# Kernel optimization log

Measured on AMD Instinct MI355X. Metric: run time of the kernel, lower is better.

The kernel has to match this reference:

```python
import jax, jax.numpy as jnp
import numpy as np

V, D, NL, K, B, L, FF = 32000, 512, 4, 32, 2, 1024, 2048


def _ln(x, g, b, eps=1e-5):
    m = jnp.mean(x, axis=-1, keepdims=True)
    v = jnp.mean((x - m) ** 2, axis=-1, keepdims=True)
    return (x - m) * jax.lax.rsqrt(v + eps) * g + b


def setup_inputs() -> dict:
    key = jax.random.key(0)
    ks = jax.random.split(key, 16)
    s = 0.02
    n = lambda k, shape: jax.random.normal(k, shape, jnp.float32) * s
    inp = {
        "tokens": jax.random.randint(ks[0], (B, L), 0, V),
        "embed": n(ks[1], (V, D)),
        "ln1_g": jnp.ones((NL, D)), "ln1_b": jnp.zeros((NL, D)),
        "cp_w1": n(ks[2], (NL, D, D)), "cp_b1": jnp.zeros((NL, D)),
        "cp_w2": n(ks[3], (NL, D, K)), "cp_b2": jnp.zeros((NL, K)),
        "pos_scale": 0.5 * jnp.ones((NL,)), "content_scale": 0.5 * jnp.ones((NL,)),
        "val_w": n(ks[4], (NL, D, D)), "val_b": jnp.zeros((NL, D)),
        "oln_g": jnp.ones((NL, D)), "oln_b": jnp.zeros((NL, D)),
        "out_w": n(ks[5], (NL, D, D)), "out_b": jnp.zeros((NL, D)),
        "ln2_g": jnp.ones((NL, D)), "ln2_b": jnp.zeros((NL, D)),
        "ffn_w1": n(ks[6], (NL, D, FF)), "ffn_b1": jnp.zeros((NL, FF)),
        "ffn_w2": n(ks[7], (NL, FF, D)), "ffn_b2": jnp.zeros((NL, D)),
        "no_g": jnp.ones((D,)), "no_b": jnp.zeros((D,)),
        "head_b": jnp.zeros((V,)),
    }
    return inp


def _forward(tokens, embed, ln1_g, ln1_b, cp_w1, cp_b1, cp_w2, cp_b2,
             pos_scale, content_scale, val_w, val_b, oln_g, oln_b, out_w, out_b,
             ln2_g, ln2_b, ffn_w1, ffn_b1, ffn_w2, ffn_b2, no_g, no_b, head_b):
    Bn, Ln = tokens.shape
    Kn = cp_b2.shape[1]
    # fixed positional phases (register_buffer in torch)
    freqs = 1.0 / 10000.0 ** (jnp.arange(Kn, dtype=jnp.float32) / Kn)
    pos_phase = jnp.arange(Ln, dtype=jnp.float32)[:, None] * freqs[None, :]  # [L,K]
    inv_norm = 1.0 / jnp.sqrt(jnp.arange(1, Ln + 1, dtype=jnp.float32) * Kn)[None, :, None]
    h = embed[tokens]  # [B,L,D]
    for i in range(ln1_g.shape[0]):
        # --- DualAddressingPhasor on normed input ---
        x = _ln(h, ln1_g[i], ln1_b[i])
        cp = jnp.tanh(jnp.tanh(x @ cp_w1[i] + cp_b1[i]) @ cp_w2[i] + cp_b2[i]) * jnp.pi  # [B,L,K]
        tp = pos_scale[i] * pos_phase[None] + content_scale[i] * cp
        v = x @ val_w[i] + val_b[i]  # [B,L,D]
        c, s_ = jnp.cos(tp), jnp.sin(tp)  # [B,L,K]
        mem_r = jnp.cumsum(c[..., None] * v[:, :, None, :], axis=1)  # [B,L,K,D]
        mem_i = jnp.cumsum(s_[..., None] * v[:, :, None, :], axis=1)
        retrieved = (jnp.einsum('blkd,blk->bld', mem_r, c)
                     + jnp.einsum('blkd,blk->bld', mem_i, s_)) * inv_norm
        # phasor returns x + to_out(retrieved); block adds it back to h
        h = h + x + (_ln(retrieved, oln_g[i], oln_b[i]) @ out_w[i] + out_b[i])
        # --- FFN ---
        y = _ln(h, ln2_g[i], ln2_b[i])
        h = h + jax.nn.gelu(y @ ffn_w1[i] + ffn_b1[i], approximate=False) @ ffn_w2[i] + ffn_b2[i]
    # tied output head: head.weight = embed.weight
    return _ln(h, no_g, no_b) @ embed.T + head_b


def reference(tokens, embed, ln1_g, ln1_b, cp_w1, cp_b1, cp_w2, cp_b2,
              pos_scale, content_scale, val_w, val_b, oln_g, oln_b, out_w, out_b,
              ln2_g, ln2_b, ffn_w1, ffn_b1, ffn_w2, ffn_b2, no_g, no_b, head_b):
    return _forward(tokens, embed, ln1_g, ln1_b, cp_w1, cp_b1, cp_w2, cp_b2,
                    pos_scale, content_scale, val_w, val_b, oln_g, oln_b, out_w, out_b,
                    ln2_g, ln2_b, ffn_w1, ffn_b1, ffn_w2, ffn_b2, no_g, no_b, head_b)
```

## Files before the change

### kernel.cpp

```cpp
#include <hip/hip_runtime.h>
#include <hip/hip_bf16.h>
#include <math.h>

#define V_  32000
#define D_  512
#define NL_ 4
#define K_  32
#define B_  2
#define L_  1024
#define FF_ 2048
#define MR_ (B_ * L_)

typedef __bf16 bf16_t;
typedef __bf16 bf16x8 __attribute__((ext_vector_type(8)));
typedef float  f32x4  __attribute__((ext_vector_type(4)));

#define FLAG_TANH   1
#define FLAG_GELU   2
#define FLAG_INV    8
#define FLAG_CAUSAL 16
#define FLAG_TANHLO 32
#define FLAG_TRI    64
#define FLAG_HALFK  128

#define GLDS(gsrc, ldst) \
  __builtin_amdgcn_global_load_lds( \
      (const __attribute__((address_space(1))) unsigned int*)(const void*)(gsrc), \
      (__attribute__((address_space(3))) unsigned int*)(void*)(ldst), 16, 0, 0)

__global__ void gather_kernel(const int* __restrict__ tokens,
                              const float* __restrict__ embed,
                              float* __restrict__ h) {
    int row = blockIdx.x;
    int t = tokens[row];
    const float4* src = (const float4*)(embed + (size_t)t * D_);
    float4* dst = (float4*)(h + (size_t)row * D_);
    dst[threadIdx.x] = src[threadIdx.x];
}

__global__ __launch_bounds__(256) void cvt_kernel(const float* __restrict__ in,
                                                  bf16_t* __restrict__ out) {
    size_t i = ((size_t)blockIdx.x * 256 + threadIdx.x) * 8;
    float4 f0 = ((const float4*)(in + i))[0];
    float4 f1 = ((const float4*)(in + i))[1];
    bf16x8 ov;
    ov[0] = (bf16_t)f0.x; ov[1] = (bf16_t)f0.y;
    ov[2] = (bf16_t)f0.z; ov[3] = (bf16_t)f0.w;
    ov[4] = (bf16_t)f1.x; ov[5] = (bf16_t)f1.y;
    ov[6] = (bf16_t)f1.z; ov[7] = (bf16_t)f1.w;
    *(bf16x8*)(out + i) = ov;
}

__global__ void bconcat_kernel(const float* __restrict__ a,
                               const float* __restrict__ b,
                               float* __restrict__ o) {
    int i = blockIdx.x, t = threadIdx.x;
    o[(size_t)i * 2 * D_ + t]       = a[(size_t)i * D_ + t];
    o[(size_t)i * 2 * D_ + D_ + t]  = b[(size_t)i * D_ + t];
}

__global__ __launch_bounds__(256) void ln_kernel(const float* __restrict__ in,
                                                 const float* __restrict__ g,
                                                 const float* __restrict__ b,
                                                 float* __restrict__ outf,
                                                 bf16_t* __restrict__ outb) {
    int row = blockIdx.x, tid = threadIdx.x;
    const float* rp = in + (size_t)row * D_;
    float v0 = rp[tid], v1 = rp[tid + 256];
    float s = v0 + v1, q = v0 * v0 + v1 * v1;
#pragma unroll
    for (int o = 32; o > 0; o >>= 1) {
        s += __shfl_down(s, o, 64);
        q += __shfl_down(q, o, 64);
    }
    __shared__ float ss[4], sq[4];
    if ((tid & 63) == 0) { ss[tid >> 6] = s; sq[tid >> 6] = q; }
    __syncthreads();
    float ts = ss[0] + ss[1] + ss[2] + ss[3];
    float tq = sq[0] + sq[1] + sq[2] + sq[3];
    float mean = ts * (1.0f / D_);
    float var = tq * (1.0f / D_) - mean * mean;
    float rstd = rsqrtf(var + 1e-5f);
    float o0 = (v0 - mean) * rstd * g[tid] + b[tid];
    float o1 = (v1 - mean) * rstd * g[tid + 256] + b[tid + 256];
    if (outf) {
        outf[(size_t)row * D_ + tid]       = o0;
        outf[(size_t)row * D_ + tid + 256] = o1;
    }
    if (outb) {
        outb[(size_t)row * D_ + tid]       = (bf16_t)o0;
        outb[(size_t)row * D_ + tid + 256] = (bf16_t)o1;
    }
}

__global__ __launch_bounds__(256) void sumk_ln_kernel(
    const float* __restrict__ p0, const float* __restrict__ p1,
    const float* __restrict__ bias, float* __restrict__ h,
    const float* __restrict__ g, const float* __restrict__ b,
    float* __restrict__ outf, bf16_t* __restrict__ outb) {
    int row = blockIdx.x, tid = threadIdx.x;
    size_t o = (size_t)row * D_;
    float v0 = h[o + tid]       + p0[o + tid]       + p1[o + tid]       + bias[tid];
    float v1 = h[o + tid + 256] + p0[o + tid + 256] + p1[o + tid + 256] + bias[tid + 256];
    h[o + tid]       = v0;
    h[o + tid + 256] = v1;
    float s = v0 + v1, q = v0 * v0 + v1 * v1;
#pragma unroll
    for (int of = 32; of > 0; of >>= 1) {
        s += __shfl_down(s, of, 64);
        q += __shfl_down(q, of, 64);
    }
    __shared__ float ss[4], sq[4];
    if ((tid & 63) == 0) { ss[tid >> 6] = s; sq[tid >> 6] = q; }
    __syncthreads();
    float ts = ss[0] + ss[1] + ss[2] + ss[3];
    float tq = sq[0] + sq[1] + sq[2] + sq[3];
    float mean = ts * (1.0f / D_);
    float var = tq * (1.0f / D_) - mean * mean;
    float rstd = rsqrtf(var + 1e-5f);
    float o0 = (v0 - mean) * rstd * g[tid] + b[tid];
    float o1 = (v1 - mean) * rstd * g[tid + 256] + b[tid + 256];
    if (outf) {
        outf[o + tid]       = o0;
        outf[o + tid + 256] = o1;
    }
    outb[o + tid]       = (bf16_t)o0;
    outb[o + tid + 256] = (bf16_t)o1;
}

__global__ __launch_bounds__(256) void tconv_kernel(const float* __restrict__ in,
                                                    bf16_t* __restrict__ out,
                                                    int R, int C,
                                                    size_t inz, size_t outz) {
    __shared__ float t[32][33];
    const float* ip = in + (size_t)blockIdx.z * inz;
    bf16_t* op = out + (size_t)blockIdx.z * outz;
    int r0 = blockIdx.y * 32, c0 = blockIdx.x * 32;
    int tx = threadIdx.x & 31, ty = threadIdx.x >> 5;
#pragma unroll
    for (int rr = 0; rr < 4; ++rr)
        t[ty + rr * 8][tx] = ip[(size_t)(r0 + ty + rr * 8) * C + c0 + tx];
    __syncthreads();
#pragma unroll
    for (int rr = 0; rr < 4; ++rr)
        op[(size_t)(c0 + ty + rr * 8) * R + r0 + tx] = (bf16_t)t[tx][ty + rr * 8];
}

template<int BM, int BN, int NBUF, int BK, bool BF32>
__global__ __launch_bounds__(256) void mgemm(
    const bf16_t* __restrict__ A, const void* __restrict__ Bp,
    const float* __restrict__ bias, const float* __restrict__ res1,
    const float* __restrict__ res2, float* __restrict__ Cf,
    bf16_t* __restrict__ Cb, int M, int N, int Kd, int flags,
    long long strA, long long strB, long long strC, int swz) {
    __shared__ bf16_t sA[NBUF][BM * BK];
    __shared__ bf16_t sB[NBUF][BN * BK];
    const int tid = threadIdx.x;
    const int wave = tid >> 6, lane = tid & 63;
    const int lrow = lane & 15, quad = lane >> 4;
    int bx = blockIdx.x, by = blockIdx.y;
    if (swz) {
        int gx = gridDim.x, gy = gridDim.y;
        int nwg = gx * gy;
        int lid = by * gx + bx;
        int q = nwg >> 3, r = nwg & 7;
        int xcd = lid & 7, slot = lid >> 3;
        int base = (xcd < r) ? xcd * (q + 1) : r * (q + 1) + (xcd - r) * q;
        int nid = base + slot;
        bx = nid / gy;
        by = nid - bx * gy;
    }
    if ((flags & FLAG_TRI) && bx > by) return;
    const int m0 = by * BM, n0 = bx * BN;
    const int z = blockIdx.z;
    A += (size_t)z * strA;
    const bf16_t* Bb = (const bf16_t*)Bp + (BF32 ? 0 : (size_t)z * strB);
    const float*  Bf = (const float*)Bp  + (BF32 ? (size_t)z * strB : 0);
    constexpr int TM = BM / 32, TN = BN / 32;
    const int wm = (wave >> 1) * (BM / 2), wn = (wave & 1) * (BN / 2);
    f32x4 acc[TM][TN] = {};

    if constexpr (BF32) {
        for (int k0 = 0; k0 < Kd; k0 += 32) {
#pragma unroll
            for (int rb = 0; rb < BM / 64; ++rb) {
                int rowblk = wave * (BM / 64) + rb;
                int ml = rowblk * 16 + (lane >> 2);
                int qs = (lane & 3) ^ ((ml >> 1) & 3);
                GLDS(A + (size_t)(m0 + ml) * Kd + k0 + qs * 8, &sA[0][rowblk * 512]);
            }
#pragma unroll
            for (int rb = 0; rb < (BN * 4) / 256; ++rb) {
                int s = rb * 256 + tid;
                int nl = s >> 2, ql = s & 3;
                int qs = ql ^ ((nl >> 1) & 3);
                const float* src = Bf + (size_t)(n0 + nl) * Kd + k0 + qs * 8;
                float4 f0 = ((const float4*)src)[0];
                float4 f1 = ((const float4*)src)[1];
                bf16x8 ov;
                ov[0] = (bf16_t)f0.x; ov[1] = (bf16_t)f0.y;
                ov[2] = (bf16_t)f0.z; ov[3] = (bf16_t)f0.w;
                ov[4] = (bf16_t)f1.x; ov[5] = (bf16_t)f1.y;
                ov[6] = (bf16_t)f1.z; ov[7] = (bf16_t)f1.w;
                *(bf16x8*)(&sB[0][s * 8]) = ov;
            }
            __syncthreads();
            bf16x8 af[TM], bv[TN];
#pragma unroll
            for (int i = 0; i < TM; ++i) {
                int row = wm + i * 16 + lrow;
                af[i] = *(const bf16x8*)(&sA[0][(row * 4 + (quad ^ ((row >> 1) & 3))) * 8]);
            }
#pragma unroll
            for (int j = 0; j < TN; ++j) {
                int rown = wn + j * 16 + lrow;
                bv[j] = *(const bf16x8*)(&sB[0][(rown * 4 + (quad ^ ((rown >> 1) & 3))) * 8]);
            }
#pragma unroll
            for (int i = 0; i < TM; ++i)
#pragma unroll
                for (int j = 0; j < TN; ++j)
                    acc[i][j] = __builtin_amdgcn_mfma_f32_16x16x32_bf16(af[i], bv[j], acc[i][j], 0, 0, 0);
            __syncthreads();
        }
    } else if constexpr (BK == 64) {
        int kend = Kd;
        if (flags & FLAG_CAUSAL) { int ke = m0 + BM; kend = ke < Kd ? ke : Kd; }
        if (flags & FLAG_HALFK) kend = Kd >> 1;
        const int nk = kend >> 6;
        constexpr int NLD = BM / 32 + BN / 32;
        auto stage = [&](int t, int buf) {
            const int k0 = t << 6;
#pragma unroll
            for (int rb = 0; rb < BM / 32; ++rb) {
                int r0 = (wave * (BM / 32) + rb) * 8;
                int row = r0 + (lane >> 3);
                int cs_ = (lane & 7) ^ (row & 7);
                GLDS(A + (size_t)(m0 + row) * Kd + k0 + cs_ * 8, &sA[buf][r0 * 64]);
            }
#pragma unroll
            for (int rb = 0; rb < BN / 32; ++rb) {
                int r0 = (wave * (BN / 32) + rb) * 8;
                int row = r0 + (lane >> 3);
                int cs_ = (lane & 7) ^ (row & 7);
                GLDS(Bb + (size_t)(n0 + row) * Kd + k0 + cs_ * 8, &sB[buf][r0 * 64]);
            }
        };
        auto compute = [&](int buf) {
            const bf16_t* sAc = sA[buf];
            const bf16_t* sBc = sB[buf];
            bf16x8 a0[TM], a1[TM], b0[TN], b1[TN];
#pragma unroll
            for (int i = 0; i < TM; ++i) {
                int row = wm + i * 16 + lrow;
                a0[i] = *(const bf16x8*)(sAc + row * 64 + ((quad       ^ (row & 7)) * 8));
                a1[i] = *(const bf16x8*)(sAc + row * 64 + (((4 | quad) ^ (row & 7)) * 8));
            }
#pragma unroll
            for (int j = 0; j < TN; ++j) {
                int rown = wn + j * 16 + lrow;
                b0[j] = *(const bf16x8*)(sBc + rown * 64 + ((quad       ^ (rown & 7)) * 8));
                b1[j] = *(const bf16x8*)(sBc + rown * 64 + (((4 | quad) ^ (rown & 7)) * 8));
            }
#pragma unroll
            for (int i = 0; i < TM; ++i)
#pragma unroll
                for (int j = 0; j < TN; ++j)
                    acc[i][j] = __builtin_amdgcn_mfma_f32_16x16x32_bf16(a0[i], b0[j], acc[i][j], 0, 0, 0);
#pragma unroll
            for (int i = 0; i < TM; ++i)
#pragma unroll
                for (int j = 0; j < TN; ++j)
                    acc[i][j] = __builtin_amdgcn_mfma_f32_16x16x32_bf16(a1[i], b1[j], acc[i][j], 0, 0, 0);
        };
        for (int t = 0; t < NBUF - 1 && t < nk; ++t) stage(t, t);
        int bcur = 0;
        for (int t = 0; t < nk; ++t) {
            const int nxt = t + NBUF - 1;
            if (nxt < nk) {
                int bn = bcur + NBUF - 1; if (bn >= NBUF) bn -= NBUF;
                stage(nxt, bn);
            }
            const int last = (nxt < nk) ? nxt : nk - 1;
            const int ahead = last - t;
            if (ahead >= 2)      asm volatile("s_waitcnt vmcnt(%0)" :: "n"(2 * NLD) : "memory");
            else if (ahead == 1) asm volatile("s_waitcnt vmcnt(%0)" :: "n"(1 * NLD) : "memory");
            else                 asm volatile("s_waitcnt vmcnt(0)" ::: "memory");
            __builtin_amdgcn_s_barrier();
            compute(bcur);
            asm volatile("s_waitcnt lgkmcnt(0)" ::: "memory");
            __builtin_amdgcn_s_barrier();
            bcur = (bcur + 1 == NBUF) ? 0 : bcur + 1;
        }
    } else {
        int kend = Kd;
        if (flags & FLAG_CAUSAL) { int ke = m0 + BM; kend = ke < Kd ? ke : Kd; }
        if (flags & FLAG_HALFK) kend = Kd >> 1;
        const int nk = kend >> 5;
        constexpr int NLD = BM / 64 + BN / 64;
        auto stage = [&](int t, int buf) {
            const int k0 = t << 5;
#pragma unroll
            for (int rb = 0; rb < BM / 64; ++rb) {
                int rowblk = wave * (BM / 64) + rb;
                int ml = rowblk * 16 + (lane >> 2);
                int qs = (lane & 3) ^ ((ml >> 1) & 3);
                GLDS(A + (size_t)(m0 + ml) * Kd + k0 + qs * 8, &sA[buf][rowblk * 512]);
            }
#pragma unroll
            for (int rb = 0; rb < BN / 64; ++rb) {
                int rowblk = wave * (BN / 64) + rb;
                int nl = rowblk * 16 + (lane >> 2);
                int qs = (lane & 3) ^ ((nl >> 1) & 3);
                GLDS(Bb + (size_t)(n0 + nl) * Kd + k0 + qs * 8, &sB[buf][rowblk * 512]);
            }
            if constexpr (BN == 64) {
                int nl = wave * 16 + (lane >> 2);
                int qs = (lane & 3) ^ ((nl >> 1) & 3);
                GLDS(Bb + (size_t)(n0 + nl) * Kd + k0 + qs * 8, &sB[buf][wave * 512]);
            }
        };
        auto compute = [&](int buf) {
            const bf16_t* sAc = sA[buf];
            const bf16_t* sBc = sB[buf];
            bf16x8 af[TM], bv[TN];
#pragma unroll
            for (int i = 0; i < TM; ++i) {
                int row = wm + i * 16 + lrow;
                af[i] = *(const bf16x8*)(sAc + (row * 4 + (quad ^ ((row >> 1) & 3))) * 8);
            }
#pragma unroll
            for (int j = 0; j < TN; ++j) {
                int rown = wn + j * 16 + lrow;
                bv[j] = *(const bf16x8*)(sBc + (rown * 4 + (quad ^ ((rown >> 1) & 3))) * 8);
            }
#pragma unroll
            for (int i = 0; i < TM; ++i)
#pragma unroll
                for (int j = 0; j < TN; ++j)
                    acc[i][j] = __builtin_amdgcn_mfma_f32_16x16x32_bf16(af[i], bv[j], acc[i][j], 0, 0, 0);
        };
        constexpr int NLDE = NLD + (BN == 64 ? 1 : 0);
        if constexpr (NBUF == 2) {
            stage(0, 0);
            int cur = 0;
            for (int t = 0; t < nk; ++t) {
                if (t + 1 < nk) {
                    stage(t + 1, cur ^ 1);
                    asm volatile("s_waitcnt vmcnt(%0)" :: "n"(NLDE) : "memory");
                } else {
                    asm volatile("s_waitcnt vmcnt(0)" ::: "memory");
                }
                __builtin_amdgcn_s_barrier();
                compute(cur);
                asm volatile("s_waitcnt lgkmcnt(0)" ::: "memory");
                __builtin_amdgcn_s_barrier();
                cur ^= 1;
            }
        } else {
            stage(0, 0);
            if (nk > 1) stage(1, 1);
            int b0 = 0;
            for (int t = 0; t < nk; ++t) {
                const int nxt = t + 2;
                if (nxt < nk) {
                    int bn = b0 + 2; if (bn >= 3) bn -= 3;
                    stage(nxt, bn);
                }
                const int last = (nxt < nk) ? nxt : nk - 1;
                const int ahead = last - t;
                if (ahead >= 2)      asm volatile("s_waitcnt vmcnt(%0)" :: "n"(2 * NLDE) : "memory");
                else if (ahead == 1) asm volatile("s_waitcnt vmcnt(%0)" :: "n"(1 * NLDE) : "memory");
                else                 asm volatile("s_waitcnt vmcnt(0)" ::: "memory");
                __builtin_amdgcn_s_barrier();
                compute(b0);
                asm volatile("s_waitcnt lgkmcnt(0)" ::: "memory");
                __builtin_amdgcn_s_barrier();
                b0 = (b0 == 2) ? 0 : b0 + 1;
            }
        }
    }

    const size_t zo = (size_t)z * strC;
#pragma unroll
    for (int i = 0; i < TM; ++i) {
#pragma unroll
        for (int reg = 0; reg < 4; ++reg) {
            int m = m0 + wm + i * 16 + quad * 4 + reg;
            float rs = (flags & FLAG_INV) ? rsqrtf((float)(m + 1) * (float)K_) : 1.0f;
#pragma unroll
            for (int j = 0; j < TN; ++j) {
                int n = n0 + wn + j * 16 + lrow;
                float vv = acc[i][j][reg];
                if (bias) vv += bias[n];
                vv *= rs;
                if (flags & FLAG_TANH) vv = tanhf(vv);
                else if (flags & FLAG_GELU) vv = 0.5f * vv * (1.0f + erff(vv * 0.7071067811865476f));
                else if (flags & FLAG_TANHLO) { if (n < D_) vv = tanhf(vv); }
                if ((flags & FLAG_TRI) && n > m) vv = 0.f;
                size_t idx = zo + (size_t)m * N + n;
                if (res1) vv += res1[idx];
                if (res2) vv += res2[idx];
                if (Cf) Cf[idx] = vv;
                if (Cb) Cb[idx] = (bf16_t)vv;
            }
        }
    }
}

__global__ __launch_bounds__(256) void phase_kernel(const float* __restrict__ t1,
                             const float* __restrict__ w2,
                             const float* __restrict__ b2,
                             const float* __restrict__ ps,
                             const float* __restrict__ cs,
                             int layer,
                             bf16_t* __restrict__ csb) {
    int tid = threadIdx.x;
    int rl = tid >> 6;
    int k = tid & 31, hh = (tid >> 5) & 1;
    int row = blockIdx.x * 4 + rl;
    int l = row & (L_ - 1);
    const float* tr = t1 + (size_t)row * (2 * D_);
    float acc = 0.f;
    for (int d = hh * 256; d < hh * 256 + 256; ++d)
        acc = fmaf(tr[d], w2[d * K_ + k], acc);
    __shared__ float red[256];
    red[tid] = acc;
    __syncthreads();
    if (hh == 0) {
        float zz = red[rl * 64 + k] + red[rl * 64 + 32 + k] + b2[k];
        float cp = tanhf(zz) * 3.14159265358979323846f;
        float freq = expf(-(float)k * (9.210340371976184f / (float)K_));
        float tp = ps[layer] * (float)l * freq + cs[layer] * cp;
        csb[(size_t)row * 64 + k]      = (bf16_t)cosf(tp);
        csb[(size_t)row * 64 + 32 + k] = (bf16_t)sinf(tp);
    }
}

extern "C" void kernel_launch(void* const* d_in, const int* in_sizes, int n_in,
                              void* d_out, int out_size, void* d_ws, size_t ws_size,
                              hipStream_t stream) {
    const int*   tokens        = (const int*)d_in[0];
    const float* embed         = (const float*)d_in[1];
    const float* ln1_g         = (const float*)d_in[2];
    const float* ln1_b         = (const float*)d_in[3];
    const float* cp_w1         = (const float*)d_in[4];
    const float* cp_b1         = (const float*)d_in[5];
    const float* cp_w2         = (const float*)d_in[6];
    const float* cp_b2         = (const float*)d_in[7];
    const float* pos_scale     = (const float*)d_in[8];
    const float* content_scale = (const float*)d_in[9];
    const float* val_w         = (const float*)d_in[10];
    const float* val_b         = (const float*)d_in[11];
    const float* oln_g         = (const float*)d_in[12];
    const float* oln_b         = (const float*)d_in[13];
    const float* out_w         = (const float*)d_in[14];
    const float* out_b         = (const float*)d_in[15];
    const float* ln2_g         = (const float*)d_in[16];
    const float* ln2_b         = (const float*)d_in[17];
    const float* ffn_w1        = (const float*)d_in[18];
    const float* ffn_b1        = (const float*)d_in[19];
    const float* ffn_w2        = (const float*)d_in[20];
    const float* ffn_b2        = (const float*)d_in[21];
    const float* no_g          = (const float*)d_in[22];
    const float* no_b          = (const float*)d_in[23];
    const float* head_b        = (const float*)d_in[24];
    float* out = (float*)d_out;

    float* h   = out;
    float* x   = h  + (size_t)MR_ * D_;
    float* t1v = x  + (size_t)MR_ * D_;
    float* r   = t1v + (size_t)MR_ * 2 * D_;
    bf16_t* x_bf  = (bf16_t*)(r + (size_t)MR_ * D_);
    bf16_t* r_bf  = x_bf  + (size_t)MR_ * D_;
    bf16_t* y_bf  = r_bf  + (size_t)MR_ * D_;
    bf16_t* ff_bf = y_bf  + (size_t)MR_ * D_;
    bf16_t* sc_bf = ff_bf + (size_t)MR_ * FF_;
    bf16_t* vT_bf = sc_bf + (size_t)B_ * L_ * L_;
    bf16_t* csb   = vT_bf + (size_t)B_ * D_ * L_;
    bf16_t* wvT   = csb   + (size_t)MR_ * 64;
    bf16_t* owT   = wvT   + (size_t)NL_ * 2 * D_ * D_;
    bf16_t* f1T   = owT   + (size_t)NL_ * D_ * D_;
    bf16_t* f2T   = f1T   + (size_t)NL_ * FF_ * D_;
    float*  b1v   = (float*)(f2T + (size_t)NL_ * D_ * FF_);
    float*  pK    = b1v + (size_t)NL_ * 2 * D_;
    bf16_t* hn_bf = (bf16_t*)d_ws;
    bf16_t* emb_bf = hn_bf + (size_t)MR_ * D_;
    const bool big_ws =
        ws_size >= ((size_t)MR_ * D_ + (size_t)V_ * D_) * sizeof(bf16_t);

    gather_kernel<<<MR_, 128, 0, stream>>>(tokens, embed, h);

    tconv_kernel<<<dim3(16, 16, NL_), 256, 0, stream>>>(cp_w1, wvT, D_, D_, (size_t)D_ * D_, (size_t)2 * D_ * D_);
    tconv_kernel<<<dim3(16, 16, NL_), 256, 0, stream>>>(val_w, wvT + (size_t)D_ * D_, D_, D_, (size_t)D_ * D_, (size_t)2 * D_ * D_);
    bconcat_kernel<<<NL_, 512, 0, stream>>>(cp_b1, val_b, b1v);
    tconv_kernel<<<dim3(16, 16, NL_), 256, 0, stream>>>(out_w, owT, D_, D_, (size_t)D_ * D_, (size_t)D_ * D_);
    tconv_kernel<<<dim3(64, 16, NL_), 256, 0, stream>>>(ffn_w1, f1T, D_, FF_, (size_t)D_ * FF_, (size_t)D_ * FF_);
    tconv_kernel<<<dim3(16, 64, NL_), 256, 0, stream>>>(ffn_w2, f2T, FF_, D_, (size_t)FF_ * D_, (size_t)FF_ * D_);
    if (big_ws)
        cvt_kernel<<<(V_ * D_) / 2048, 256, 0, stream>>>(embed, emb_bf);

    for (int i = 0; i < NL_; ++i) {
        if (i == 0)
            ln_kernel<<<MR_, 256, 0, stream>>>(h, ln1_g, ln1_b, x, x_bf);
        mgemm<64, 64, 3, 64, false><<<dim3(16, 32, 1), 256, 0, stream>>>(
            x_bf, wvT + (size_t)i * 2 * D_ * D_, b1v + (size_t)i * 2 * D_,
            nullptr, nullptr, t1v, nullptr, MR_, 2 * D_, D_, FLAG_TANHLO, 0, 0, 0, 1);
        phase_kernel<<<MR_ / 4, 256, 0, stream>>>(
            t1v, cp_w2 + (size_t)i * D_ * K_, cp_b2 + i * K_,
            pos_scale, content_scale, i, csb);
        tconv_kernel<<<dim3(16, 32, B_), 256, 0, stream>>>(
            t1v + D_, vT_bf, L_, 2 * D_, (size_t)L_ * 2 * D_, (size_t)D_ * L_);
        mgemm<64, 64, 3, 64, false><<<dim3(L_ / 64, L_ / 64, B_), 256, 0, stream>>>(
            csb, csb, nullptr, nullptr, nullptr, nullptr, sc_bf,
            L_, L_, 64, FLAG_TRI,
            (long long)L_ * 64, (long long)L_ * 64, (long long)L_ * L_, 0);
        mgemm<64, 64, 3, 64, false><<<dim3(8, 16, B_), 256, 0, stream>>>(
            sc_bf, vT_bf, nullptr, nullptr, nullptr, r, nullptr,
            L_, D_, L_, FLAG_INV | FLAG_CAUSAL,
            (long long)L_ * L_, (long long)D_ * L_, (long long)L_ * D_, 1);
        ln_kernel<<<MR_, 256, 0, stream>>>(r, oln_g + i * D_, oln_b + i * D_, nullptr, r_bf);
        mgemm<64, 64, 3, 64, false><<<dim3(8, 32, 1), 256, 0, stream>>>(
            r_bf, owT + (size_t)i * D_ * D_, out_b + i * D_,
            h, x, h, nullptr, MR_, D_, D_, 0, 0, 0, 0, 1);
        ln_kernel<<<MR_, 256, 0, stream>>>(h, ln2_g + i * D_, ln2_b + i * D_, nullptr, y_bf);
        mgemm<64, 64, 3, 64, false><<<dim3(32, 32, 1), 256, 0, stream>>>(
            y_bf, f1T + (size_t)i * FF_ * D_, ffn_b1 + i * FF_,
            nullptr, nullptr, nullptr, ff_bf, MR_, FF_, D_, FLAG_GELU, 0, 0, 0, 1);
        mgemm<64, 64, 3, 64, false><<<dim3(8, 32, 2), 256, 0, stream>>>(
            ff_bf, f2T + (size_t)i * D_ * FF_, nullptr,
            nullptr, nullptr, pK, nullptr, MR_, D_, FF_, FLAG_HALFK,
            (long long)(FF_ / 2), (long long)(FF_ / 2), (long long)MR_ * D_, 1);
        if (i < NL_ - 1) {
            sumk_ln_kernel<<<MR_, 256, 0, stream>>>(
                pK, pK + (size_t)MR_ * D_, ffn_b2 + i * D_, h,
                ln1_g + (i + 1) * D_, ln1_b + (i + 1) * D_, x, x_bf);
        } else {
            sumk_ln_kernel<<<MR_, 256, 0, stream>>>(
                pK, pK + (size_t)MR_ * D_, ffn_b2 + i * D_, h,
                no_g, no_b, nullptr, hn_bf);
        }
    }

    if (big_ws) {
        mgemm<128, 64, 3, 32, false><<<dim3(V_ / 64, MR_ / 128, 1), 256, 0, stream>>>(
            hn_bf, emb_bf, head_b, nullptr, nullptr, out, nullptr,
            MR_, V_, D_, 0, 0, 0, 0, 1);
    } else {
        mgemm<128, 128, 1, 32, true><<<dim3(V_ / 128, MR_ / 128, 1), 256, 0, stream>>>(
            hn_bf, embed, head_b, nullptr, nullptr, out, nullptr,
            MR_, V_, D_, 0, 0, 0, 0, 1);
    }
}
```

Baseline: 1.318 ms.

## Fuse phasor score and value GEMMs into one flash-style causal attention kernel

Replaces the two-GEMM path (materialise the triangular LxL score matrix in bf16, then multiply by V) with a single kernel. Each block computes a 64x64 score tile in registers, masks it causally, stages it through shared memory, and accumulates it against V tiles, with the inverse-norm scaling done in the epilogue. This removes the global write and re-read of the score matrix and one launch per layer. The cost is recomputing score tiles once per D-tile (eight times), with a single-buffered loop that has no prefetching. Separately, the out-projection and FFN2 GEMMs switch to 64x32 tiles with twice as many blocks, to raise occupancy on the N=512 outputs.

```diff
diff --git a/kernel.cpp b/kernel.cpp
--- a/kernel.cpp
+++ b/kernel.cpp
@@ -144,6 +144,103 @@
 #pragma unroll
     for (int rr = 0; rr < 4; ++rr)
         op[(size_t)(c0 + ty + rr * 8) * R + r0 + tx] = (bf16_t)t[tx][ty + rr * 8];
+}
+
+__global__ __launch_bounds__(256) void phattn_kernel(
+    const bf16_t* __restrict__ csb,
+    const bf16_t* __restrict__ vT,
+    float* __restrict__ r) {
+    __shared__ bf16_t sQ[64 * 64];
+    __shared__ bf16_t sK[64 * 64];
+    __shared__ bf16_t sV[64 * 64];
+    __shared__ bf16_t sS[64][72];
+    const int tid = threadIdx.x;
+    const int wave = tid >> 6, lane = tid & 63;
+    const int lrow = lane & 15, quad = lane >> 4;
+    const int wm = (wave >> 1) * 32, wn = (wave & 1) * 32;
+    const int b = blockIdx.z;
+    const int m0 = blockIdx.y * 64, d0 = blockIdx.x * 64;
+    const bf16_t* cs = csb + (size_t)b * L_ * 64;
+    const bf16_t* vz = vT + (size_t)b * D_ * L_;
+#pragma unroll
+    for (int p = 0; p < 2; ++p) {
+        int s = p * 256 + tid;
+        int row = s >> 3, c8 = s & 7;
+        *(bf16x8*)(sQ + row * 64 + c8 * 8) =
+            *(const bf16x8*)(cs + (size_t)(m0 + row) * 64 + c8 * 8);
+    }
+    f32x4 racc[2][2] = {};
+    const int njt = (m0 >> 6) + 1;
+    for (int jt = 0; jt < njt; ++jt) {
+        const int j0 = jt * 64;
+        __syncthreads();
+#pragma unroll
+        for (int p = 0; p < 2; ++p) {
+            int s = p * 256 + tid;
+            int row = s >> 3, c8 = s & 7;
+            *(bf16x8*)(sK + row * 64 + c8 * 8) =
+                *(const bf16x8*)(cs + (size_t)(j0 + row) * 64 + c8 * 8);
+            *(bf16x8*)(sV + row * 64 + c8 * 8) =
+                *(const bf16x8*)(vz + (size_t)(d0 + row) * L_ + j0 + c8 * 8);
+        }
+        __syncthreads();
+        f32x4 sacc[2][2] = {};
+#pragma unroll
+        for (int ks = 0; ks < 2; ++ks) {
+            bf16x8 qa[2], kb[2];
+#pragma unroll
+            for (int i = 0; i < 2; ++i)
+                qa[i] = *(const bf16x8*)(sQ + (wm + i * 16 + lrow) * 64 + ks * 32 + quad * 8);
+#pragma unroll
+            for (int j = 0; j < 2; ++j)
+                kb[j] = *(const bf16x8*)(sK + (wn + j * 16 + lrow) * 64 + ks * 32 + quad * 8);
+#pragma unroll
+            for (int i = 0; i < 2; ++i)
+#pragma unroll
+                for (int j = 0; j < 2; ++j)
+                    sacc[i][j] = __builtin_amdgcn_mfma_f32_16x16x32_bf16(qa[i], kb[j], sacc[i][j], 0, 0, 0);
+        }
+#pragma unroll
+        for (int i = 0; i < 2; ++i)
+#pragma unroll
+            for (int reg = 0; reg < 4; ++reg)
+#pragma unroll
+                for (int j = 0; j < 2; ++j) {
+                    int mm = wm + i * 16 + quad * 4 + reg;
+                    int jj = wn + j * 16 + lrow;
+                    float vv = sacc[i][j][reg];
+                    if (j0 + jj > m0 + mm) vv = 0.f;
+                    sS[mm][jj] = (bf16_t)vv;
+                }
+        __syncthreads();
+#pragma unroll
+        for (int ks = 0; ks < 2; ++ks) {
+            bf16x8 pa[2], vb[2];
+#pragma unroll
+            for (int i = 0; i < 2; ++i)
+                pa[i] = *(const bf16x8*)(&sS[wm + i * 16 + lrow][ks * 32 + quad * 8]);
+#pragma unroll
+            for (int j = 0; j < 2; ++j)
+                vb[j] = *(const bf16x8*)(sV + (wn + j * 16 + lrow) * 64 + ks * 32 + quad * 8);
+#pragma unroll
+            for (int i = 0; i < 2; ++i)
+#pragma unroll
+                for (int j = 0; j < 2; ++j)
+                    racc[i][j] = __builtin_amdgcn_mfma_f32_16x16x32_bf16(pa[i], vb[j], racc[i][j], 0, 0, 0);
+        }
+    }
+#pragma unroll
+    for (int i = 0; i < 2; ++i)
+#pragma unroll
+        for (int reg = 0; reg < 4; ++reg) {
+            int m = m0 + wm + i * 16 + quad * 4 + reg;
+            float rs = rsqrtf((float)(m + 1) * (float)K_);
+#pragma unroll
+            for (int j = 0; j < 2; ++j) {
+                int d = d0 + wn + j * 16 + lrow;
+                r[(size_t)b * L_ * D_ + (size_t)m * D_ + d] = racc[i][j][reg] * rs;
+            }
+        }
 }
 
 template<int BM, int BN, int NBUF, int BK, bool BF32>
@@ -511,23 +608,17 @@
             pos_scale, content_scale, i, csb);
         tconv_kernel<<<dim3(16, 32, B_), 256, 0, stream>>>(
             t1v + D_, vT_bf, L_, 2 * D_, (size_t)L_ * 2 * D_, (size_t)D_ * L_);
-        mgemm<64, 64, 3, 64, false><<<dim3(L_ / 64, L_ / 64, B_), 256, 0, stream>>>(
-            csb, csb, nullptr, nullptr, nullptr, nullptr, sc_bf,
-            L_, L_, 64, FLAG_TRI,
-            (long long)L_ * 64, (long long)L_ * 64, (long long)L_ * L_, 0);
-        mgemm<64, 64, 3, 64, false><<<dim3(8, 16, B_), 256, 0, stream>>>(
-            sc_bf, vT_bf, nullptr, nullptr, nullptr, r, nullptr,
-            L_, D_, L_, FLAG_INV | FLAG_CAUSAL,
-            (long long)L_ * L_, (long long)D_ * L_, (long long)L_ * D_, 1);
+        phattn_kernel<<<dim3(D_ / 64, L_ / 64, B_), 256, 0, stream>>>(
+            csb, vT_bf, r);
         ln_kernel<<<MR_, 256, 0, stream>>>(r, oln_g + i * D_, oln_b + i * D_, nullptr, r_bf);
-        mgemm<64, 64, 3, 64, false><<<dim3(8, 32, 1), 256, 0, stream>>>(
+        mgemm<64, 32, 3, 64, false><<<dim3(16, 32, 1), 256, 0, stream>>>(
             r_bf, owT + (size_t)i * D_ * D_, out_b + i * D_,
             h, x, h, nullptr, MR_, D_, D_, 0, 0, 0, 0, 1);
         ln_kernel<<<MR_, 256, 0, stream>>>(h, ln2_g + i * D_, ln2_b + i * D_, nullptr, y_bf);
         mgemm<64, 64, 3, 64, false><<<dim3(32, 32, 1), 256, 0, stream>>>(
             y_bf, f1T + (size_t)i * FF_ * D_, ffn_b1 + i * FF_,
             nullptr, nullptr, nullptr, ff_bf, MR_, FF_, D_, FLAG_GELU, 0, 0, 0, 1);
-        mgemm<64, 64, 3, 64, false><<<dim3(8, 32, 2), 256, 0, stream>>>(
+        mgemm<64, 32, 3, 64, false><<<dim3(16, 32, 2), 256, 0, stream>>>(
             ff_bf, f2T + (size_t)i * D_ * FF_, nullptr,
             nullptr, nullptr, pK, nullptr, MR_, D_, FF_, FLAG_HALFK,
             (long long)(FF_ / 2), (long long)(FF_ / 2), (long long)MR_ * D_, 1);
```

After: 1.312 ms. No clear change (-0.4%).
